# Optimization experiments

Hardware: AMD Instinct MI355X
Metric: run time of the kernel (lower is better)

## Reference

```python
import jax, jax.numpy as jnp
import numpy as np

B, D, M, H = 512, 2048, 128, 128
INIT_SCALE = 0.02

def setup_inputs() -> dict:
    key = jax.random.key(0)
    k_x, k_w1, k_w2 = jax.random.split(key, 3)
    return {
        "pre_activation_history": jax.random.normal(k_x, (B, D, M), dtype=jnp.float32),
        # conv1: grouped Conv1d(D -> D*H, kernel=M, groups=D) == per-channel W1[d]: [H, M]
        "W1": jax.random.normal(k_w1, (D, H, M), dtype=jnp.float32) * INIT_SCALE,
        "b1": jnp.zeros((D, H), dtype=jnp.float32),
        # linear_out: grouped 1x1 Conv1d(D*H -> D, groups=D) == per-channel w2[d]: [H]
        "W2": jax.random.normal(k_w2, (D, H), dtype=jnp.float32) * INIT_SCALE,
        "b2": jnp.zeros((D,), dtype=jnp.float32),
    }

def reference(pre_activation_history, W1, b1, W2, b2):
    # per-neuron MLP: [B,D,M] x [D,H,M] -> [B,D,H]
    h = jnp.einsum("bdm,dhm->bdh", pre_activation_history, W1) + b1
    g = jax.nn.gelu(h, approximate=False)  # torch F.gelu default = exact erf
    out = jnp.einsum("bdh,dh->bd", g, W2) + b2  # [B, D]
    return out
```

## Files before the change

kernel.cpp:

```cpp
#include <hip/hip_runtime.h>
#include <hip/hip_bf16.h>
#include <math.h>

#define B_SZ 512
#define D_SZ 2048
#define M_SZ 128
#define H_SZ 128
#define BCHUNK 64
#define NCHUNKS (B_SZ / BCHUNK)

typedef __attribute__((ext_vector_type(8))) short bf16x8;
typedef __attribute__((ext_vector_type(4))) float f32x4;
typedef __attribute__((ext_vector_type(4))) unsigned short us4;

__device__ __forceinline__ unsigned short f2bf(float f) {
    unsigned u = __builtin_bit_cast(unsigned, f);
    u += 0x7fffu + ((u >> 16) & 1u);
    return (unsigned short)(u >> 16);
}

__global__ __launch_bounds__(256, 3) void nlm_kernel(
    const float* __restrict__ x,
    const float* __restrict__ W1,
    const float* __restrict__ b1,
    const float* __restrict__ W2,
    const float* __restrict__ b2,
    float* __restrict__ out)
{
    __shared__ __align__(16) unsigned short W1s[H_SZ * M_SZ];
    __shared__ __align__(16) unsigned short Xs[BCHUNK * M_SZ];
    __shared__ float w2s[H_SZ];
    __shared__ float b1s[H_SZ];
    __shared__ float red[2][BCHUNK];

    const int bid = blockIdx.x;
    const int d = (bid & 7) * 256 + (bid >> 3);

    const int tid  = threadIdx.x;
    const int l    = tid & 63;
    const int w    = tid >> 6;
    const int wr   = w >> 1;
    const int wc   = w & 1;
    const int lrow = l & 15;
    const int lk   = l >> 4;
    const int swz  = (lrow & 7) << 4;

    const float* W1d = W1 + (size_t)d * (H_SZ * M_SZ);
    #pragma unroll
    for (int i = 0; i < 16; ++i) {
        int idx = tid + i * 256;
        int r = idx >> 5, c4 = idx & 31;
        const float4 v = *(const float4*)(W1d + (r << 7) + (c4 << 2));
        us4 u; u.x = f2bf(v.x); u.y = f2bf(v.y); u.z = f2bf(v.z); u.w = f2bf(v.w);
        int byte = (r << 8) + ((c4 << 3) ^ ((r & 7) << 4));
        *(us4*)((char*)W1s + byte) = u;
    }
    if (tid < H_SZ) {
        w2s[tid] = W2[(size_t)d * H_SZ + tid];
        b1s[tid] = b1[(size_t)d * H_SZ + tid];
    }
    const float b2v = b2[d];

    const int xr_row = tid >> 5;
    const int xr_c4  = tid & 31;
    float4 xr[8];
    #pragma unroll
    for (int i = 0; i < 8; ++i)
        xr[i] = *(const float4*)(x + ((size_t)(xr_row + i * 8) * D_SZ + d) * M_SZ + (xr_c4 << 2));

    for (int c = 0; c < NCHUNKS; ++c) {
        #pragma unroll
        for (int i = 0; i < 8; ++i) {
            int r = xr_row + i * 8;
            us4 u; u.x = f2bf(xr[i].x); u.y = f2bf(xr[i].y);
                   u.z = f2bf(xr[i].z); u.w = f2bf(xr[i].w);
            int byte = (r << 8) + ((xr_c4 << 3) ^ ((r & 7) << 4));
            *(us4*)((char*)Xs + byte) = u;
        }
        __syncthreads();

        if (c + 1 < NCHUNKS) {
            const size_t b0n = (size_t)(c + 1) * BCHUNK;
            #pragma unroll
            for (int i = 0; i < 8; ++i)
                xr[i] = *(const float4*)(x + ((b0n + xr_row + i * 8) * D_SZ + d) * M_SZ + (xr_c4 << 2));
        }

        f32x4 acc[2][4];
        #pragma unroll
        for (int m = 0; m < 2; ++m)
            #pragma unroll
            for (int n = 0; n < 4; ++n)
                acc[m][n] = (f32x4){0.f, 0.f, 0.f, 0.f};

        #pragma unroll
        for (int k = 0; k < 4; ++k) {
            const int colb = (k << 6) + (lk << 4);
            bf16x8 a[2], bb[4];
            #pragma unroll
            for (int m = 0; m < 2; ++m) {
                int row = wr * 32 + m * 16 + lrow;
                a[m] = *(const bf16x8*)((const char*)Xs + (row << 8) + (colb ^ swz));
            }
            #pragma unroll
            for (int n = 0; n < 4; ++n) {
                int row = wc * 64 + n * 16 + lrow;
                bb[n] = *(const bf16x8*)((const char*)W1s + (row << 8) + (colb ^ swz));
            }
            #pragma unroll
            for (int m = 0; m < 2; ++m)
                #pragma unroll
                for (int n = 0; n < 4; ++n)
                    acc[m][n] = __builtin_amdgcn_mfma_f32_16x16x32_bf16(a[m], bb[n], acc[m][n], 0, 0, 0);
        }

        float p[2][4];
        #pragma unroll
        for (int m = 0; m < 2; ++m)
            #pragma unroll
            for (int r = 0; r < 4; ++r)
                p[m][r] = 0.f;

        #pragma unroll
        for (int n = 0; n < 4; ++n) {
            const int cn = wc * 64 + n * 16 + lrow;
            const float w2v = w2s[cn];
            const float b1v = b1s[cn];
            #pragma unroll
            for (int m = 0; m < 2; ++m)
                #pragma unroll
                for (int r = 0; r < 4; ++r) {
                    float h = acc[m][n][r] + b1v;
                    float g = 0.5f * h * (1.0f + erff(h * 0.70710678118654752f));
                    p[m][r] += g * w2v;
                }
        }

        #pragma unroll
        for (int off = 1; off < 16; off <<= 1)
            #pragma unroll
            for (int m = 0; m < 2; ++m)
                #pragma unroll
                for (int r = 0; r < 4; ++r)
                    p[m][r] += __shfl_xor(p[m][r], off, 64);

        if (lrow == 0) {
            #pragma unroll
            for (int m = 0; m < 2; ++m)
                #pragma unroll
                for (int r = 0; r < 4; ++r)
                    red[wc][wr * 32 + m * 16 + lk * 4 + r] = p[m][r];
        }
        __syncthreads();

        if (tid < BCHUNK) {
            float v = red[0][tid] + red[1][tid] + b2v;
            out[(size_t)(c * BCHUNK + tid) * D_SZ + d] = v;
        }
    }
}

extern "C" void kernel_launch(void* const* d_in, const int* in_sizes, int n_in,
                              void* d_out, int out_size, void* d_ws, size_t ws_size,
                              hipStream_t stream) {
    const float* x  = (const float*)d_in[0];
    const float* W1 = (const float*)d_in[1];
    const float* b1 = (const float*)d_in[2];
    const float* W2 = (const float*)d_in[3];
    const float* b2 = (const float*)d_in[4];
    float* out = (float*)d_out;

    hipLaunchKernelGGL(nlm_kernel, dim3(D_SZ), dim3(256), 0, stream,
                       x, W1, b1, W2, b2, out);
}
```

Baseline: 146.8 us.

## Replace erf GELU with tanh-approx, give each wave full H, drop LDS reduction

Swaps the exact erf GELU for a tanh-style approximation written as x*sigmoid(1.5958x+0.0714x^3), using a fast exp and a fast divide. Each wave now owns 16 batch rows across all 128 hidden units, so the cross-wave LDS reduction and the second __syncthreads go away. W2 and b1 now sit in registers instead of shared memory. A raw s_barrier after the MFMA loop protects the Xs buffer before the next chunk overwrites it. The approximation moves results away from the exact-erf reference and could exceed tolerance. Each wave also loads eight B fragments per k step, which adds LDS traffic.

```diff
diff --git a/kernel.cpp b/kernel.cpp
--- a/kernel.cpp
+++ b/kernel.cpp
@@ -19,6 +19,13 @@
     return (unsigned short)(u >> 16);
 }
 
+__device__ __forceinline__ float gelu_fast(float h) {
+    float u = h * h;
+    float z = h * fmaf(0.0713548162726f, u, 1.5957691216057308f);
+    float e = __expf(-z);
+    return __fdividef(h, 1.0f + e);
+}
+
 __global__ __launch_bounds__(256, 3) void nlm_kernel(
     const float* __restrict__ x,
     const float* __restrict__ W1,
@@ -29,9 +36,6 @@
 {
     __shared__ __align__(16) unsigned short W1s[H_SZ * M_SZ];
     __shared__ __align__(16) unsigned short Xs[BCHUNK * M_SZ];
-    __shared__ float w2s[H_SZ];
-    __shared__ float b1s[H_SZ];
-    __shared__ float red[2][BCHUNK];
 
     const int bid = blockIdx.x;
     const int d = (bid & 7) * 256 + (bid >> 3);
@@ -39,8 +43,6 @@
     const int tid  = threadIdx.x;
     const int l    = tid & 63;
     const int w    = tid >> 6;
-    const int wr   = w >> 1;
-    const int wc   = w & 1;
     const int lrow = l & 15;
     const int lk   = l >> 4;
     const int swz  = (lrow & 7) << 4;
@@ -55,9 +57,12 @@
         int byte = (r << 8) + ((c4 << 3) ^ ((r & 7) << 4));
         *(us4*)((char*)W1s + byte) = u;
     }
-    if (tid < H_SZ) {
-        w2s[tid] = W2[(size_t)d * H_SZ + tid];
-        b1s[tid] = b1[(size_t)d * H_SZ + tid];
+
+    float w2r[8], b1r[8];
+    #pragma unroll
+    for (int n = 0; n < 8; ++n) {
+        w2r[n] = W2[(size_t)d * H_SZ + n * 16 + lrow];
+        b1r[n] = b1[(size_t)d * H_SZ + n * 16 + lrow];
     }
     const float b2v = b2[d];
 
@@ -86,76 +91,55 @@
                 xr[i] = *(const float4*)(x + ((b0n + xr_row + i * 8) * D_SZ + d) * M_SZ + (xr_c4 << 2));
         }
 
-        f32x4 acc[2][4];
+        f32x4 acc[8];
         #pragma unroll
-        for (int m = 0; m < 2; ++m)
-            #pragma unroll
-            for (int n = 0; n < 4; ++n)
-                acc[m][n] = (f32x4){0.f, 0.f, 0.f, 0.f};
+        for (int n = 0; n < 8; ++n)
+            acc[n] = (f32x4){0.f, 0.f, 0.f, 0.f};
 
         #pragma unroll
         for (int k = 0; k < 4; ++k) {
             const int colb = (k << 6) + (lk << 4);
-            bf16x8 a[2], bb[4];
+            const int arow = w * 16 + lrow;
+            bf16x8 a = *(const bf16x8*)((const char*)Xs + (arow << 8) + (colb ^ swz));
+            bf16x8 bb[8];
             #pragma unroll
-            for (int m = 0; m < 2; ++m) {
-                int row = wr * 32 + m * 16 + lrow;
-                a[m] = *(const bf16x8*)((const char*)Xs + (row << 8) + (colb ^ swz));
-            }
-            #pragma unroll
-            for (int n = 0; n < 4; ++n) {
-                int row = wc * 64 + n * 16 + lrow;
+            for (int n = 0; n < 8; ++n) {
+                int row = n * 16 + lrow;
                 bb[n] = *(const bf16x8*)((const char*)W1s + (row << 8) + (colb ^ swz));
             }
             #pragma unroll
-            for (int m = 0; m < 2; ++m)
-                #pragma unroll
-                for (int n = 0; n < 4; ++n)
-                    acc[m][n] = __builtin_amdgcn_mfma_f32_16x16x32_bf16(a[m], bb[n], acc[m][n], 0, 0, 0);
+            for (int n = 0; n < 8; ++n)
+                acc[n] = __builtin_amdgcn_mfma_f32_16x16x32_bf16(a, bb[n], acc[n], 0, 0, 0);
         }
 
-        float p[2][4];
+        asm volatile("" ::: "memory");
+        __builtin_amdgcn_sched_barrier(0);
+        __builtin_amdgcn_s_barrier();
+        __builtin_amdgcn_sched_barrier(0);
+        asm volatile("" ::: "memory");
+
+        float p[4] = {0.f, 0.f, 0.f, 0.f};
         #pragma unroll
-        for (int m = 0; m < 2; ++m)
+        for (int n = 0; n < 8; ++n) {
+            const float w2v = w2r[n];
+            const float b1v = b1r[n];
             #pragma unroll
-            for (int r = 0; r < 4; ++r)
-                p[m][r] = 0.f;
-
-        #pragma unroll
-        for (int n = 0; n < 4; ++n) {
-            const int cn = wc * 64 + n * 16 + lrow;
-            const float w2v = w2s[cn];
-            const float b1v = b1s[cn];
-            #pragma unroll
-            for (int m = 0; m < 2; ++m)
-                #pragma unroll
-                for (int r = 0; r < 4; ++r) {
-                    float h = acc[m][n][r] + b1v;
-                    float g = 0.5f * h * (1.0f + erff(h * 0.70710678118654752f));
-                    p[m][r] += g * w2v;
-                }
+            for (int r = 0; r < 4; ++r) {
+                float h = acc[n][r] + b1v;
+                p[r] += gelu_fast(h) * w2v;
+            }
         }
 
         #pragma unroll
         for (int off = 1; off < 16; off <<= 1)
             #pragma unroll
-            for (int m = 0; m < 2; ++m)
-                #pragma unroll
-                for (int r = 0; r < 4; ++r)
-                    p[m][r] += __shfl_xor(p[m][r], off, 64);
+            for (int r = 0; r < 4; ++r)
+                p[r] += __shfl_xor(p[r], off, 64);
 
         if (lrow == 0) {
             #pragma unroll
-            for (int m = 0; m < 2; ++m)
-                #pragma unroll
-                for (int r = 0; r < 4; ++r)
-                    red[wc][wr * 32 + m * 16 + lk * 4 + r] = p[m][r];
-        }
-        __syncthreads();
-
-        if (tid < BCHUNK) {
-            float v = red[0][tid] + red[1][tid] + b2v;
-            out[(size_t)(c * BCHUNK + tid) * D_SZ + d] = v;
+            for (int r = 0; r < 4; ++r)
+                out[(size_t)(c * BCHUNK + w * 16 + lk * 4 + r) * D_SZ + d] = p[r] + b2v;
         }
     }
 }
```

Measured after the change: 152.3 us. 1.04x slower.

## Double batch chunk with 512-thread blocks, fast GELU, register-held bias and weights

Applied to the files above, without the earlier changes.

Each block now uses 512 threads (8 waves) and processes 128 batch rows per chunk, which halves the number of chunk iterations and barriers per channel. The exact erf GELU is replaced by a sigmoid-based tanh approximation using __expf and __fdividef. W2 and b1 values now live in registers instead of LDS. __syncthreads is replaced by an explicit lgkmcnt wait plus s_barrier. The goal is more in-flight memory traffic and less ALU time in the epilogue. The cost is roughly 1e-3 deviation from exact erf GELU and different LDS occupancy per CU.

```diff
diff --git a/kernel.cpp b/kernel.cpp
--- a/kernel.cpp
+++ b/kernel.cpp
@@ -6,7 +6,7 @@
 #define D_SZ 2048
 #define M_SZ 128
 #define H_SZ 128
-#define BCHUNK 64
+#define BCHUNK 128
 #define NCHUNKS (B_SZ / BCHUNK)
 
 typedef __attribute__((ext_vector_type(8))) short bf16x8;
@@ -19,7 +19,22 @@
     return (unsigned short)(u >> 16);
 }
 
-__global__ __launch_bounds__(256, 3) void nlm_kernel(
+__device__ __forceinline__ float gelu_fast(float h) {
+    float u = h * h;
+    float z = h * fmaf(0.0713548162726f, u, 1.5957691216057308f);
+    float e = __expf(-z);
+    return __fdividef(h, 1.0f + e);
+}
+
+__device__ __forceinline__ void lds_barrier() {
+    __builtin_amdgcn_sched_barrier(0);
+    asm volatile("s_waitcnt lgkmcnt(0)" ::: "memory");
+    __builtin_amdgcn_sched_barrier(0);
+    __builtin_amdgcn_s_barrier();
+    __builtin_amdgcn_sched_barrier(0);
+}
+
+__global__ __launch_bounds__(512, 4) void nlm_kernel(
     const float* __restrict__ x,
     const float* __restrict__ W1,
     const float* __restrict__ b1,
@@ -29,8 +44,6 @@
 {
     __shared__ __align__(16) unsigned short W1s[H_SZ * M_SZ];
     __shared__ __align__(16) unsigned short Xs[BCHUNK * M_SZ];
-    __shared__ float w2s[H_SZ];
-    __shared__ float b1s[H_SZ];
     __shared__ float red[2][BCHUNK];
 
     const int bid = blockIdx.x;
@@ -47,17 +60,21 @@
 
     const float* W1d = W1 + (size_t)d * (H_SZ * M_SZ);
     #pragma unroll
-    for (int i = 0; i < 16; ++i) {
-        int idx = tid + i * 256;
+    for (int i = 0; i < 8; ++i) {
+        int idx = tid + i * 512;
         int r = idx >> 5, c4 = idx & 31;
         const float4 v = *(const float4*)(W1d + (r << 7) + (c4 << 2));
         us4 u; u.x = f2bf(v.x); u.y = f2bf(v.y); u.z = f2bf(v.z); u.w = f2bf(v.w);
         int byte = (r << 8) + ((c4 << 3) ^ ((r & 7) << 4));
         *(us4*)((char*)W1s + byte) = u;
     }
-    if (tid < H_SZ) {
-        w2s[tid] = W2[(size_t)d * H_SZ + tid];
-        b1s[tid] = b1[(size_t)d * H_SZ + tid];
+
+    float w2r[4], b1r[4];
+    #pragma unroll
+    for (int n = 0; n < 4; ++n) {
+        int hh = wc * 64 + n * 16 + lrow;
+        w2r[n] = W2[(size_t)d * H_SZ + hh];
+        b1r[n] = b1[(size_t)d * H_SZ + hh];
     }
     const float b2v = b2[d];
 
@@ -66,24 +83,24 @@
     float4 xr[8];
     #pragma unroll
     for (int i = 0; i < 8; ++i)
-        xr[i] = *(const float4*)(x + ((size_t)(xr_row + i * 8) * D_SZ + d) * M_SZ + (xr_c4 << 2));
+        xr[i] = *(const float4*)(x + ((size_t)(xr_row + i * 16) * D_SZ + d) * M_SZ + (xr_c4 << 2));
 
     for (int c = 0; c < NCHUNKS; ++c) {
         #pragma unroll
         for (int i = 0; i < 8; ++i) {
-            int r = xr_row + i * 8;
+            int r = xr_row + i * 16;
             us4 u; u.x = f2bf(xr[i].x); u.y = f2bf(xr[i].y);
                    u.z = f2bf(xr[i].z); u.w = f2bf(xr[i].w);
             int byte = (r << 8) + ((xr_c4 << 3) ^ ((r & 7) << 4));
             *(us4*)((char*)Xs + byte) = u;
         }
-        __syncthreads();
+        lds_barrier();
 
         if (c + 1 < NCHUNKS) {
             const size_t b0n = (size_t)(c + 1) * BCHUNK;
             #pragma unroll
             for (int i = 0; i < 8; ++i)
-                xr[i] = *(const float4*)(x + ((b0n + xr_row + i * 8) * D_SZ + d) * M_SZ + (xr_c4 << 2));
+                xr[i] = *(const float4*)(x + ((b0n + xr_row + i * 16) * D_SZ + d) * M_SZ + (xr_c4 << 2));
         }
 
         f32x4 acc[2][4];
@@ -123,16 +140,14 @@
 
         #pragma unroll
         for (int n = 0; n < 4; ++n) {
-            const int cn = wc * 64 + n * 16 + lrow;
-            const float w2v = w2s[cn];
-            const float b1v = b1s[cn];
+            const float w2v = w2r[n];
+            const float b1v = b1r[n];
             #pragma unroll
             for (int m = 0; m < 2; ++m)
                 #pragma unroll
                 for (int r = 0; r < 4; ++r) {
                     float h = acc[m][n][r] + b1v;
-                    float g = 0.5f * h * (1.0f + erff(h * 0.70710678118654752f));
-                    p[m][r] += g * w2v;
+                    p[m][r] += gelu_fast(h) * w2v;
                 }
         }
 
@@ -151,7 +166,7 @@
                 for (int r = 0; r < 4; ++r)
                     red[wc][wr * 32 + m * 16 + lk * 4 + r] = p[m][r];
         }
-        __syncthreads();
+        lds_barrier();
 
         if (tid < BCHUNK) {
             float v = red[0][tid] + red[1][tid] + b2v;
@@ -170,6 +185,6 @@
     const float* b2 = (const float*)d_in[4];
     float* out = (float*)d_out;
 
-    hipLaunchKernelGGL(nlm_kernel, dim3(D_SZ), dim3(256), 0, stream,
+    hipLaunchKernelGGL(nlm_kernel, dim3(D_SZ), dim3(512), 0, stream,
                        x, W1, b1, W2, b2, out);
 }
```

Result: slower. 188.6 us (+28.5%).

## Use LDS-only barriers, fast tanh-form GELU, and deferred batched output stores

Applied to the files above, without the earlier changes.

Replaces __syncthreads with a barrier that waits only on LDS counters (lgkmcnt), so prefetched global loads of the next x chunk can stay in flight across the barrier. Swaps exact erf GELU for the tanh approximation written in sigmoid form with __expf and a fast divide, which cuts ALU work in the epilogue but adds approximation error. Output values are staged in shared memory and written once at the end by all 256 threads rather than by 64 threads per chunk. Extra LDS use could lower occupancy slightly.

```diff
diff --git a/kernel.cpp b/kernel.cpp
--- a/kernel.cpp
+++ b/kernel.cpp
@@ -19,6 +19,21 @@
     return (unsigned short)(u >> 16);
 }
 
+__device__ __forceinline__ float gelu_fast(float h) {
+    float u = h * h;
+    float z = h * fmaf(0.0713548162726f, u, 1.5957691216057308f);
+    float e = __expf(-z);
+    return __fdividef(h, 1.0f + e);
+}
+
+__device__ __forceinline__ void lds_barrier() {
+    __builtin_amdgcn_sched_barrier(0);
+    asm volatile("s_waitcnt lgkmcnt(0)" ::: "memory");
+    __builtin_amdgcn_sched_barrier(0);
+    __builtin_amdgcn_s_barrier();
+    __builtin_amdgcn_sched_barrier(0);
+}
+
 __global__ __launch_bounds__(256, 3) void nlm_kernel(
     const float* __restrict__ x,
     const float* __restrict__ W1,
@@ -32,6 +47,7 @@
     __shared__ float w2s[H_SZ];
     __shared__ float b1s[H_SZ];
     __shared__ float red[2][BCHUNK];
+    __shared__ float outLDS[B_SZ];
 
     const int bid = blockIdx.x;
     const int d = (bid & 7) * 256 + (bid >> 3);
@@ -77,7 +93,7 @@
             int byte = (r << 8) + ((xr_c4 << 3) ^ ((r & 7) << 4));
             *(us4*)((char*)Xs + byte) = u;
         }
-        __syncthreads();
+        lds_barrier();
 
         if (c + 1 < NCHUNKS) {
             const size_t b0n = (size_t)(c + 1) * BCHUNK;
@@ -131,8 +147,7 @@
                 #pragma unroll
                 for (int r = 0; r < 4; ++r) {
                     float h = acc[m][n][r] + b1v;
-                    float g = 0.5f * h * (1.0f + erff(h * 0.70710678118654752f));
-                    p[m][r] += g * w2v;
+                    p[m][r] += gelu_fast(h) * w2v;
                 }
         }
 
@@ -151,12 +166,18 @@
                 for (int r = 0; r < 4; ++r)
                     red[wc][wr * 32 + m * 16 + lk * 4 + r] = p[m][r];
         }
-        __syncthreads();
+        lds_barrier();
 
-        if (tid < BCHUNK) {
-            float v = red[0][tid] + red[1][tid] + b2v;
-            out[(size_t)(c * BCHUNK + tid) * D_SZ + d] = v;
-        }
+        if (tid < BCHUNK)
+            outLDS[c * BCHUNK + tid] = red[0][tid] + red[1][tid] + b2v;
+    }
+
+    lds_barrier();
+    {
+        float v0 = outLDS[tid]       + 0.0f;
+        float v1 = outLDS[tid + 256] + 0.0f;
+        out[(size_t)tid * D_SZ + d]         = v0;
+        out[(size_t)(tid + 256) * D_SZ + d] = v1;
     }
 }
 
```

Measured after the change: 153.0 us. 1.04x slower.
